# Kernel optimization log

Hardware: AMD Instinct MI355X
Metric: run time of the kernel (lower is better)

Reference implementation:

```python
import jax, jax.numpy as jnp
import numpy as np

GRID_SIZE, SPLINE_ORDER = 5, 3
NUM_BASES = GRID_SIZE + SPLINE_ORDER  # 8
GRID = jnp.asarray(np.arange(-SPLINE_ORDER, GRID_SIZE + SPLINE_ORDER + 1, dtype=np.float32) * (2.0 / GRID_SIZE) - 1.0)  # (12,)


def _b_splines(x):
    # x: (M, F) -> (M, F, NUM_BASES), Cox-de Boor recursion on shared uniform grid
    g = GRID
    xe = x[..., None]
    b = ((xe >= g[:-1]) & (xe < g[1:])).astype(x.dtype)
    for k in range(1, SPLINE_ORDER + 1):
        b = ((xe - g[:-(k + 1)]) / (g[k:-1] - g[:-(k + 1)]) * b[..., :-1]
             + (g[k + 1:] - xe) / (g[k + 1:] - g[1:-k]) * b[..., 1:])
    return b


def _kan_linear(x, base_w, spline_w):
    # x: (M, Fin); base_w: (Fout, Fin); spline_w: (Fout, Fin, NUM_BASES)
    base = jax.nn.silu(x) @ base_w.T
    spl = _b_splines(x).reshape(x.shape[0], -1) @ spline_w.reshape(spline_w.shape[0], -1).T
    return base + spl


def _ln(x, g, b, eps=1e-5):
    mu = jnp.mean(x, -1, keepdims=True)
    var = jnp.var(x, -1, keepdims=True)
    return (x - mu) * jax.lax.rsqrt(var + eps) * g + b


def _dwconv(img, w, b):
    C = img.shape[1]
    out = jax.lax.conv_general_dilated(img, w, (1, 1), 'SAME',
        dimension_numbers=('NCHW', 'OIHW', 'NCHW'), feature_group_count=C)
    return out + b[None, :, None, None]


def _dw_bn_relu(x, H, W, w, b, gamma, beta, eps=1e-5):
    # BN in eval mode with running_mean=0, running_var=1
    B, N, C = x.shape
    img = x.transpose(0, 2, 1).reshape(B, C, H, W)
    out = _dwconv(img, w, b)
    out = out * (gamma * (1.0 / np.sqrt(1.0 + eps)))[None, :, None, None] + beta[None, :, None, None]
    out = jax.nn.relu(out)
    return out.reshape(B, C, H * W).transpose(0, 2, 1)


def _cross_selective_scan(img, x_proj_w, dt_w, dt_b, A_logs, Ds, g, b):
    # img: (B, Di, H, W). 4-direction diagonal/antidiagonal selective scan (VMamba-style).
    B, Di, H, W = img.shape
    L = H * W
    K = x_proj_w.shape[0]
    R = dt_w.shape[2]
    Nst = A_logs.shape[1]
    i = jnp.arange(H)[:, None]
    j = jnp.arange(W)[None, :]
    diag = (i + j) % W
    adiag = (j - i) % W
    diag_inv = (jnp.arange(W)[None, :] - i) % W
    adiag_inv = (jnp.arange(W)[None, :] + i) % W

    def gather(x, idx):
        gth = jnp.take_along_axis(x, idx[None, None], axis=3)  # (B,Di,H,W)
        return gth.transpose(0, 1, 3, 2).reshape(B, Di, L)

    def scatter(flat, idx_inv):
        v = flat.reshape(B, Di, W, H).transpose(0, 1, 3, 2)
        return jnp.take_along_axis(v, idx_inv[None, None], axis=3)

    gd, gad = gather(img, diag), gather(img, adiag)
    xs = jnp.stack([gd, gad, jnp.flip(gd, -1), jnp.flip(gad, -1)], axis=1)  # (B,K,Di,L)
    x_dbl = jnp.einsum('bkdl,kcd->bkcl', xs, x_proj_w)
    dts, Bs, Cs = jnp.split(x_dbl, [R, R + Nst], axis=2)  # (B,K,R,L),(B,K,N,L),(B,K,N,L)
    dts = jnp.einsum('bkrl,kdr->bkdl', dts, dt_w)
    delta = jax.nn.softplus(dts + dt_b[None, :, :, None])  # (B,K,Di,L)
    A = -jnp.exp(A_logs).reshape(K, Di, Nst)

    def step(hst, inp):
        u_t, d_t, B_t, C_t = inp  # (B,K,Di),(B,K,Di),(B,K,N),(B,K,N)
        dA = jnp.exp(d_t[..., None] * A)
        hst = dA * hst + (d_t * u_t)[..., None] * B_t[:, :, None, :]
        return hst, jnp.einsum('bkdn,bkn->bkd', hst, C_t)

    h0 = jnp.zeros((B, K, Di, Nst), img.dtype)
    _, ys = jax.lax.scan(step, h0,
        (xs.transpose(3, 0, 1, 2), delta.transpose(3, 0, 1, 2),
         Bs.transpose(3, 0, 1, 2), Cs.transpose(3, 0, 1, 2)))  # ys: (L,B,K,Di)
    ys = ys.transpose(1, 2, 3, 0) + Ds.reshape(K, Di)[None, :, :, None] * xs  # (B,K,Di,L)
    yd = ys[:, 0] + jnp.flip(ys[:, 2], -1)
    ya = ys[:, 1] + jnp.flip(ys[:, 3], -1)
    y = scatter(yd, diag_inv) + scatter(ya, adiag_inv)  # (B,Di,H,W)
    y = y.reshape(B, Di, L).transpose(0, 2, 1)
    return _ln(y, g, b)  # (B,L,Di)


def setup_inputs():
    key = jax.random.key(0)
    ks = iter(jax.random.split(key, 48))
    B, H, W, C = 4, 64, 64, 96
    Di, K, Nst = 2 * C, 4, 16
    R = int(np.ceil(C / 16))
    L = H * W

    def rn(shape, s=0.05):
        return jax.random.normal(next(ks), shape, jnp.float32) * s

    return dict(
        x=jax.random.normal(next(ks), (B, L, C), jnp.float32),
        H=H, W=W,
        norm1_g=jnp.ones((C,), jnp.float32), norm1_b=jnp.zeros((C,), jnp.float32),
        in_proj_w=rn((2 * Di, C)),
        conv_w=rn((Di, 1, 3, 3), 0.2), conv_b=jnp.zeros((Di,), jnp.float32),
        x_proj_w=rn((K, R + 2 * Nst, Di)),
        dt_w=rn((K, Di, R), 0.1), dt_b=rn((K, Di), 0.1),
        A_logs=jax.random.uniform(next(ks), (K * Di, Nst), jnp.float32),
        Ds=jnp.ones((K * Di,), jnp.float32),
        out_norm_g=jnp.ones((Di,), jnp.float32), out_norm_b=jnp.zeros((Di,), jnp.float32),
        out_proj_w=rn((C, Di)),
        norm2_g=jnp.ones((C,), jnp.float32), norm2_b=jnp.zeros((C,), jnp.float32),
        fc1_base_w=rn((C, C)), fc1_spline_w=rn((C, C, NUM_BASES), 0.02),
        fc2_base_w=rn((C, C)), fc2_spline_w=rn((C, C, NUM_BASES), 0.02),
        fc3_base_w=rn((C, C)), fc3_spline_w=rn((C, C, NUM_BASES), 0.02),
        dw1_w=rn((C, 1, 3, 3), 0.2), dw1_b=jnp.zeros((C,), jnp.float32),
        dw1_g=jnp.ones((C,), jnp.float32), dw1_beta=jnp.zeros((C,), jnp.float32),
        dw2_w=rn((C, 1, 3, 3), 0.2), dw2_b=jnp.zeros((C,), jnp.float32),
        dw2_g=jnp.ones((C,), jnp.float32), dw2_beta=jnp.zeros((C,), jnp.float32),
        dw3_w=rn((C, 1, 3, 3), 0.2), dw3_b=jnp.zeros((C,), jnp.float32),
        dw3_g=jnp.ones((C,), jnp.float32), dw3_beta=jnp.zeros((C,), jnp.float32),
    )


def reference(x, H, W, norm1_g, norm1_b, in_proj_w, conv_w, conv_b, x_proj_w,
              dt_w, dt_b, A_logs, Ds, out_norm_g, out_norm_b, out_proj_w,
              norm2_g, norm2_b, fc1_base_w, fc1_spline_w, fc2_base_w, fc2_spline_w,
              fc3_base_w, fc3_spline_w, dw1_w, dw1_b, dw1_g, dw1_beta,
              dw2_w, dw2_b, dw2_g, dw2_beta, dw3_w, dw3_b, dw3_g, dw3_beta):
    B, L, C = x.shape
    # --- SS2D branch ---
    h = _ln(x, norm1_g, norm1_b)
    xz = h @ in_proj_w.T  # (B,L,2*Di)
    Di = xz.shape[-1] // 2
    xin, z = xz[..., :Di], xz[..., Di:]
    img = xin.transpose(0, 2, 1).reshape(B, Di, H, W)
    img = jax.nn.silu(_dwconv(img, conv_w, conv_b))
    y = _cross_selective_scan(img, x_proj_w, dt_w, dt_b, A_logs, Ds, out_norm_g, out_norm_b)
    y = y * jax.nn.silu(z)
    x = x + y @ out_proj_w.T
    # --- KAN branch ---
    h = _ln(x, norm2_g, norm2_b)
    M = B * L
    t = _kan_linear(h.reshape(M, C), fc1_base_w, fc1_spline_w).reshape(B, L, -1)
    t = _dw_bn_relu(t, H, W, dw1_w, dw1_b, dw1_g, dw1_beta)
    t = _kan_linear(t.reshape(M, -1), fc2_base_w, fc2_spline_w).reshape(B, L, -1)
    t = _dw_bn_relu(t, H, W, dw2_w, dw2_b, dw2_g, dw2_beta)
    t = _kan_linear(t.reshape(M, -1), fc3_base_w, fc3_spline_w).reshape(B, L, -1)
    t = _dw_bn_relu(t, H, W, dw3_w, dw3_b, dw3_g, dw3_beta)
    return x + t
```

## Files before the change

kernel.cpp:

```cpp
#include <hip/hip_runtime.h>
#include <math.h>

constexpr int B_  = 4;
constexpr int H_  = 64;
constexpr int W_  = 64;
constexpr int C_  = 96;
constexpr int L_  = H_ * W_;
constexpr int DI  = 192;
constexpr int K_  = 4;
constexpr int NST = 16;
constexpr int R_  = 6;
constexpr int M_  = B_ * L_;

constexpr int NCH = 128;
constexpr int CL  = 32;
constexpr int DG  = 12;

constexpr int KANK = 864;
constexpr int KLAY = 96 * KANK;

typedef __attribute__((ext_vector_type(8))) short short8;
typedef __attribute__((ext_vector_type(4))) float floatx4;
typedef __attribute__((ext_vector_type(4))) unsigned short ushort4v;

__device__ __forceinline__ float wave_sum64(float v) {
#pragma unroll
  for (int off = 1; off < 64; off <<= 1) v += __shfl_xor(v, off, 64);
  return v;
}

__device__ __forceinline__ float exp2_hw(float x) {
  return __builtin_amdgcn_exp2f(x);
}

__device__ __forceinline__ int pos_kl(int k, int l) {
  int ll = (k >= 2) ? (L_ - 1 - l) : l;
  int i = ll & 63;
  int j = ll >> 6;
  int col = ((k & 1) == 0) ? ((i + j) & 63) : ((j - i) & 63);
  return (i << 6) + col;
}

__device__ __forceinline__ int pos_pair(int pr, int ll) {
  int i = ll & 63, j = ll >> 6;
  int col = (pr == 0) ? ((i + j) & 63) : ((j - i) & 63);
  return (i << 6) + col;
}

__device__ __forceinline__ float silu_f(float x) {
  return x / (1.f + __expf(-x));
}

__device__ __forceinline__ float softplus_fast(float s) {
  return fmaxf(s, 0.f) + __logf(1.f + __expf(-fabsf(s)));
}

__device__ __forceinline__ unsigned short f2bf(float f) {
  unsigned u = __float_as_uint(f);
  unsigned r = (u + 0x7FFFu + ((u >> 16) & 1u)) >> 16;
  return (unsigned short)r;
}

__device__ __forceinline__ float bf2f(unsigned short h) {
  return __uint_as_float(((unsigned)h) << 16);
}

__device__ __forceinline__ void spline8(float x, float* bb ) {
#pragma unroll
  for (int i2 = 0; i2 < 11; i2++) {
    float g0 = 0.4f * i2 - 2.2f;
    float g1 = 0.4f * i2 - 1.8f;
    bb[i2] = (x >= g0 && x < g1) ? 1.f : 0.f;
  }
#pragma unroll
  for (int k2 = 1; k2 <= 3; k2++) {
    float invd = 1.f / (0.4f * k2);
#pragma unroll
    for (int i2 = 0; i2 + k2 < 11; i2++) {
      float gi   = 0.4f * i2 - 2.2f;
      float gik1 = 0.4f * (i2 + k2 + 1) - 2.2f;
      bb[i2] = (x - gi) * invd * bb[i2] + (gik1 - x) * invd * bb[i2 + 1];
    }
  }
}

__global__ __launch_bounds__(256) void ln96_kernel(const float* __restrict__ in,
    const float* __restrict__ g, const float* __restrict__ b,
    float* __restrict__ out) {
  int wave = blockIdx.x * 4 + (threadIdx.x >> 6);
  int lane = threadIdx.x & 63;
  const float* rp = in + (size_t)wave * C_;
  float v0 = rp[lane];
  float v1 = (lane < C_ - 64) ? rp[lane + 64] : 0.f;
  float s  = wave_sum64(v0 + v1);
  float s2 = wave_sum64(v0 * v0 + v1 * v1);
  float mean = s * (1.f / C_);
  float var  = s2 * (1.f / C_) - mean * mean;
  float inv  = rsqrtf(var + 1e-5f);
  float* op = out + (size_t)wave * C_;
  op[lane] = (v0 - mean) * inv * g[lane] + b[lane];
  if (lane < C_ - 64) op[lane + 64] = (v1 - mean) * inv * g[lane + 64] + b[lane + 64];
}

__global__ __launch_bounds__(256) void prep_inproj_kernel(const float* __restrict__ w,
    unsigned short* __restrict__ wio) {
  int idx = blockIdx.x * 256 + threadIdx.x;
  if (idx >= 384 * 96) return;
  float v = w[idx];
  unsigned short hh = f2bf(v);
  wio[idx] = hh;
  wio[36864 + idx] = f2bf(v - bf2f(hh));
}

__global__ __launch_bounds__(256) void prep_a2_kernel(const float* __restrict__ A_logs,
    float* __restrict__ a2g) {
  int idx = blockIdx.x * 256 + threadIdx.x;
  if (idx < K_ * DI * NST) a2g[idx] = -__expf(A_logs[idx]) * 1.44269504f;
}

__global__ __launch_bounds__(256) void gemm_in_mfma_kernel(const float* __restrict__ h,
    const unsigned short* __restrict__ wio, float* __restrict__ xin,
    float* __restrict__ z) {
  __shared__ __align__(16) unsigned short Wh[96][104];
  __shared__ __align__(16) unsigned short Wl[96][104];
  int row0 = blockIdx.x * 64;
  int tid = threadIdx.x;
  int wv = tid >> 6, lane = tid & 63, mrow = lane & 15, quad = lane >> 4;

  short8 ah[3], al[3];
  const float* hr = h + (size_t)(row0 + wv * 16 + mrow) * C_;
#pragma unroll
  for (int ks = 0; ks < 3; ks++) {
    float4 va = *(const float4*)&hr[ks * 32 + quad * 8];
    float4 vb = *(const float4*)&hr[ks * 32 + quad * 8 + 4];
    float f[8] = {va.x, va.y, va.z, va.w, vb.x, vb.y, vb.z, vb.w};
    short8 hh, ll;
#pragma unroll
    for (int q = 0; q < 8; q++) {
      unsigned short hv = f2bf(f[q]);
      hh[q] = (short)hv;
      ll[q] = (short)f2bf(f[q] - bf2f(hv));
    }
    ah[ks] = hh; al[ks] = ll;
  }
  for (int nc = 0; nc < 4; nc++) {
    if (nc) __syncthreads();
    for (int t = tid; t < 96 * 12; t += 256) {
      int j = t / 12, u = t % 12;
      *(short8*)&Wh[j][u * 8] = *(const short8*)&wio[(size_t)(nc * 96 + j) * 96 + u * 8];
      *(short8*)&Wl[j][u * 8] = *(const short8*)&wio[(size_t)(384 + nc * 96 + j) * 96 + u * 8];
    }
    __syncthreads();
    floatx4 acc[6];
#pragma unroll
    for (int q = 0; q < 6; q++) acc[q] = (floatx4)(0.f);
#pragma unroll
    for (int ks = 0; ks < 3; ks++) {
#pragma unroll
      for (int nt = 0; nt < 6; nt++) {
        short8 bh = *(const short8*)&Wh[nt * 16 + mrow][ks * 32 + quad * 8];
        short8 bl = *(const short8*)&Wl[nt * 16 + mrow][ks * 32 + quad * 8];
        acc[nt] = __builtin_amdgcn_mfma_f32_16x16x32_bf16(ah[ks], bh, acc[nt], 0, 0, 0);
        acc[nt] = __builtin_amdgcn_mfma_f32_16x16x32_bf16(al[ks], bh, acc[nt], 0, 0, 0);
        acc[nt] = __builtin_amdgcn_mfma_f32_16x16x32_bf16(ah[ks], bl, acc[nt], 0, 0, 0);
      }
    }
#pragma unroll
    for (int nt = 0; nt < 6; nt++) {
      int j = nc * 96 + nt * 16 + mrow;
#pragma unroll
      for (int rg = 0; rg < 4; rg++) {
        int row = row0 + wv * 16 + quad * 4 + rg;
        float v = acc[nt][rg];
        if (j < DI) xin[(size_t)row * DI + j] = v;
        else        z[(size_t)row * DI + (j - DI)] = v;
      }
    }
  }
}

__global__ __launch_bounds__(192) void conv_silu_kernel(const float* __restrict__ xin,
    const float* __restrict__ cw, const float* __restrict__ cb, float* __restrict__ imgT) {
  int p = blockIdx.x;
  int b = p >> 12;
  int ij = p & 4095;
  int i = ij >> 6, j = ij & 63;
  int c = threadIdx.x;
  float acc = cb[c];
#pragma unroll
  for (int di = -1; di <= 1; di++) {
    int ii = i + di;
    if (ii < 0 || ii >= H_) continue;
#pragma unroll
    for (int dj = -1; dj <= 1; dj++) {
      int jj = j + dj;
      if (jj < 0 || jj >= W_) continue;
      acc += xin[((size_t)b * L_ + ii * W_ + jj) * DI + c] * cw[c * 9 + (di + 1) * 3 + (dj + 1)];
    }
  }
  imgT[(size_t)p * DI + c] = silu_f(acc);
}

__global__ __launch_bounds__(256) void xdbl_mfma_kernel(const float* __restrict__ imgT,
    const float* __restrict__ xpw, float* __restrict__ dts_g,
    float* __restrict__ BsT, float* __restrict__ CsT) {
  __shared__ __align__(16) unsigned short Ah[64][104];
  __shared__ __align__(16) unsigned short Al[64][104];
  __shared__ __align__(16) unsigned short Wh[48][104];
  __shared__ __align__(16) unsigned short Wl[48][104];
  __shared__ int pos_s[64];

  int blk = blockIdx.x;
  int lt = blk & 63;
  int bk = blk >> 6;
  int k = bk % K_, b = bk / K_;
  int l0 = lt * 64;
  int tid = threadIdx.x;
  int wid = tid >> 6;
  int lane = tid & 63;
  int mrow = lane & 15, quad = lane >> 4;

  if (tid < 64) pos_s[tid] = pos_kl(k, l0 + tid);
  __syncthreads();

  floatx4 acc[3];
#pragma unroll
  for (int q = 0; q < 3; q++) acc[q] = (floatx4)(0.f);

  const float* img_b = imgT + (size_t)b * L_ * DI;
// ... 13 lines not shown
      }
      *(ushort4v*)&Ah[li][c4] = h4;
      *(ushort4v*)&Al[li][c4] = l4;
    }
    for (int t = tid; t < 48 * 24; t += 256) {
      int j = t / 24, c4 = (t % 24) * 4;
      ushort4v h4 = (ushort4v)0, l4 = (ushort4v)0;
      if (j < 38) {
        int c = (j < 32) ? (j + 6) : (j - 32);
        const float4 v = *(const float4*)&xpw[((size_t)(k * 38 + c)) * DI + kc * 96 + c4];
        float fv[4] = {v.x, v.y, v.z, v.w};
#pragma unroll
        for (int q = 0; q < 4; q++) {
          unsigned short hh = f2bf(fv[q]);
          h4[q] = hh;
          l4[q] = f2bf(fv[q] - bf2f(hh));
        }
      }
      *(ushort4v*)&Wh[j][c4] = h4;
      *(ushort4v*)&Wl[j][c4] = l4;
    }
    __syncthreads();
#pragma unroll
    for (int ks = 0; ks < 3; ks++) {
      short8 ah = *(const short8*)&Ah[wid * 16 + mrow][ks * 32 + quad * 8];
      short8 al = *(const short8*)&Al[wid * 16 + mrow][ks * 32 + quad * 8];
#pragma unroll
      for (int nt = 0; nt < 3; nt++) {
        short8 bh = *(const short8*)&Wh[nt * 16 + mrow][ks * 32 + quad * 8];
        short8 bl = *(const short8*)&Wl[nt * 16 + mrow][ks * 32 + quad * 8];
        acc[nt] = __builtin_amdgcn_mfma_f32_16x16x32_bf16(ah, bh, acc[nt], 0, 0, 0);
        acc[nt] = __builtin_amdgcn_mfma_f32_16x16x32_bf16(al, bh, acc[nt], 0, 0, 0);
        acc[nt] = __builtin_amdgcn_mfma_f32_16x16x32_bf16(ah, bl, acc[nt], 0, 0, 0);
      }
    }
  }
  size_t bkL = (size_t)(b * K_ + k) * L_ + l0;
#pragma unroll
  for (int rg = 0; rg < 4; rg++) {
    int grow = wid * 16 + quad * 4 + rg;
    size_t base = (bkL + grow) * NST;
    BsT[base + mrow] = acc[0][rg];
    CsT[base + mrow] = acc[1][rg];
    if (mrow < R_) dts_g[(bkL + grow) * 8 + mrow] = acc[2][rg];
  }
}

__global__ __launch_bounds__(192) void scan1_kernel(const float* __restrict__ imgT,
    const float* __restrict__ dts_g, const float* __restrict__ BsT,
    const float* __restrict__ a2g, const float* __restrict__ dtw,
    const float* __restrict__ dtb, float* __restrict__ hend,
    float* __restrict__ aprod) {
  __shared__ float bs_s[CL][NST];
  __shared__ float dt_s[CL][8];
  int blk = blockIdx.x;
  int c = blk % NCH;
  int tmp = blk / NCH;
  int k = tmp % K_, b = tmp / K_;
  int l0 = c * CL;
  int d = threadIdx.x;
  const float* img_b = imgT + (size_t)b * L_ * DI;
  {
    const float* Bs_bk = BsT + ((size_t)(b * K_ + k) * L_ + l0) * NST;
    for (int t = d; t < CL * NST; t += 192) bs_s[t >> 4][t & 15] = Bs_bk[t];
    const float* Dt = dts_g + ((size_t)(b * K_ + k) * L_ + l0) * 8;
    for (int t = d; t < CL * 8; t += 192) dt_s[t >> 3][t & 7] = Dt[t];
  }
  float A2[NST];
  {
    const floatx4* ap = (const floatx4*)(a2g + (size_t)(k * DI + d) * NST);
#pragma unroll
    for (int i = 0; i < 4; i++) {
      floatx4 v = ap[i];
      A2[4 * i] = v[0]; A2[4 * i + 1] = v[1]; A2[4 * i + 2] = v[2]; A2[4 * i + 3] = v[3];
    }
  }
  float w6[6], bias;
  {
    const float* wp = dtw + ((size_t)k * DI + d) * R_;
#pragma unroll
    for (int r = 0; r < 6; r++) w6[r] = wp[r];
    bias = dtb[k * DI + d];
  }
  float u[CL];
#pragma unroll
  for (int q = 0; q < CL; q++)
    u[q] = img_b[(size_t)pos_kl(k, l0 + q) * DI + d];
  __syncthreads();
  float dc[CL];
  float sum_dlt = 0.f;
#pragma unroll
  for (int q = 0; q < CL; q++) {
    const floatx4* dp = (const floatx4*)&dt_s[q][0];
    floatx4 d0 = dp[0], d1 = dp[1];
    float s = bias + w6[0] * d0[0] + w6[1] * d0[1] + w6[2] * d0[2]
                   + w6[3] * d0[3] + w6[4] * d1[0] + w6[5] * d1[1];
    dc[q] = softplus_fast(s);
    sum_dlt += dc[q];
  }
  float h[NST];
#pragma unroll
  for (int n = 0; n < NST; n++) h[n] = 0.f;
#pragma unroll
  for (int q = 0; q < CL; q++) {
    float du = dc[q] * u[q];
    floatx4 bsv[4];
    const floatx4* bp = (const floatx4*)&bs_s[q][0];
#pragma unroll
    for (int i = 0; i < 4; i++) bsv[i] = bp[i];
#pragma unroll
    for (int n = 0; n < NST; n++) {
      float dA = exp2_hw(dc[q] * A2[n]);
      h[n] = dA * h[n] + du * bsv[n >> 2][n & 3];
    }
  }
  size_t base = ((size_t)(b * K_ + k) * NCH + c) * (DI * NST) + d;
#pragma unroll
  for (int n = 0; n < NST; n++) {
    hend[base + (size_t)n * DI]  = h[n];
    aprod[base + (size_t)n * DI] = exp2_hw(A2[n] * sum_dlt);
  }
}

__global__ __launch_bounds__(256) void scan_carry_kernel(float* __restrict__ hend,
    const float* __restrict__ aprod) {
  constexpr int PF = 8;
  int blk = blockIdx.x;
  int part = blk % DG;
  int bk = blk / DG;
  const size_t DNS = (size_t)DI * NST;
  size_t base = (size_t)bk * NCH * DNS + (size_t)part * 256 + threadIdx.x;
  float hb[PF], ab[PF];
#pragma unroll
  for (int q = 0; q < PF; q++) {
    hb[q] = hend[base + (size_t)q * DNS];
    ab[q] = aprod[base + (size_t)q * DNS];
  }
  float carry = 0.f;
  for (int c0 = 0; c0 < NCH; c0 += PF) {
    float hn[PF], an[PF];
    if (c0 + PF < NCH) {
#pragma unroll
      for (int q = 0; q < PF; q++) {
        hn[q] = hend[base + (size_t)(c0 + PF + q) * DNS];
        an[q] = aprod[base + (size_t)(c0 + PF + q) * DNS];
      }
    } else {
#pragma unroll
      for (int q = 0; q < PF; q++) { hn[q] = 0.f; an[q] = 0.f; }
    }
#pragma unroll
    for (int q = 0; q < PF; q++) {
      hend[base + (size_t)(c0 + q) * DNS] = carry;
      carry = ab[q] * carry + hb[q];
    }
#pragma unroll
    for (int q = 0; q < PF; q++) { hb[q] = hn[q]; ab[q] = an[q]; }
  }
}

__global__ __launch_bounds__(192) void scan2_pair_kernel(const float* __restrict__ imgT,
    const float* __restrict__ dts_g, const float* __restrict__ BsT,
    const float* __restrict__ CsT, const float* __restrict__ a2g,
    const float* __restrict__ dtw, const float* __restrict__ dtb,
    const float* __restrict__ Ds, const float* __restrict__ carry_in,
    float* __restrict__ y02, float* __restrict__ y13) {
  __shared__ float bsf[CL][NST], csf[CL][NST], bsr[CL][NST], csr[CL][NST];
  __shared__ float dtf[CL][8], dtr[CL][8];
  int blk = blockIdx.x;
  int c  = blk % NCH;
  int pr = (blk / NCH) & 1;
  int b  = blk / (2 * NCH);
  int kf = pr, kr = pr + 2;
  int p0 = c * CL;
  int d = threadIdx.x;
  const float* img_b = imgT + (size_t)b * L_ * DI;
  {
    const float* Bf = BsT + ((size_t)(b * K_ + kf) * L_ + p0) * NST;
    const float* Cf = CsT + ((size_t)(b * K_ + kf) * L_ + p0) * NST;
    for (int t = d; t < CL * NST; t += 192) {
      bsf[t >> 4][t & 15] = Bf[t];
      csf[t >> 4][t & 15] = Cf[t];
    }
    const float* Br = BsT + (size_t)(b * K_ + kr) * L_ * NST;
    const float* Cr = CsT + (size_t)(b * K_ + kr) * L_ * NST;
    for (int t = d; t < CL * NST; t += 192) {
      int q = t >> 4, n = t & 15;
      size_t sr = (size_t)(L_ - 1 - p0 - q) * NST + n;
      bsr[q][n] = Br[sr];
      csr[q][n] = Cr[sr];
    }
    const float* Df = dts_g + ((size_t)(b * K_ + kf) * L_ + p0) * 8;
    for (int t = d; t < CL * 8; t += 192) dtf[t >> 3][t & 7] = Df[t];
    const float* Dr = dts_g + (size_t)(b * K_ + kr) * L_ * 8;
    for (int t = d; t < CL * 8; t += 192) {
      int q = t >> 3, r = t & 7;
      dtr[q][r] = Dr[(size_t)(L_ - 1 - p0 - q) * 8 + r];
    }
  }
  float u[CL], y[CL];
#pragma unroll
  for (int q = 0; q < CL; q++)
    u[q] = img_b[(size_t)pos_pair(pr, p0 + q) * DI + d];
  float dsum = 0.f;
  if (pr == 0) dsum = Ds[d] + Ds[DI + d] + Ds[2 * DI + d] + Ds[3 * DI + d];
#pragma unroll
  for (int q = 0; q < CL; q++) y[q] = dsum * u[q];
  __syncthreads();
  float A2[NST], h[NST], w6[6], bias, dc[CL];
  {
    const floatx4* ap = (const floatx4*)(a2g + (size_t)(kf * DI + d) * NST);
#pragma unroll
    for (int i = 0; i < 4; i++) {
      floatx4 v = ap[i];
      A2[4 * i] = v[0]; A2[4 * i + 1] = v[1]; A2[4 * i + 2] = v[2]; A2[4 * i + 3] = v[3];
    }
    size_t cb = ((size_t)(b * K_ + kf) * NCH + c) * (DI * NST) + d;
#pragma unroll
    for (int n = 0; n < NST; n++) h[n] = carry_in[cb + (size_t)n * DI];
    const float* wp = dtw + ((size_t)kf * DI + d) * R_;
#pragma unroll
    for (int r = 0; r < 6; r++) w6[r] = wp[r];
    bias = dtb[kf * DI + d];
  }
#pragma unroll
  for (int q = 0; q < CL; q++) {
    const floatx4* dp = (const floatx4*)&dtf[q][0];
    floatx4 d0 = dp[0], d1 = dp[1];
    float s = bias + w6[0] * d0[0] + w6[1] * d0[1] + w6[2] * d0[2]
                   + w6[3] * d0[3] + w6[4] * d1[0] + w6[5] * d1[1];
    dc[q] = softplus_fast(s);
  }
#pragma unroll
  for (int q = 0; q < CL; q++) {
    float du = dc[q] * u[q];
    floatx4 bsv[4], csv[4];
    const floatx4* bp = (const floatx4*)&bsf[q][0];
    const floatx4* cp = (const floatx4*)&csf[q][0];
#pragma unroll
    for (int i = 0; i < 4; i++) { bsv[i] = bp[i]; csv[i] = cp[i]; }
    float yq = y[q];
#pragma unroll
    for (int n = 0; n < NST; n++) {
      float dA = exp2_hw(dc[q] * A2[n]);
      h[n] = dA * h[n] + du * bsv[n >> 2][n & 3];
      yq += h[n] * csv[n >> 2][n & 3];
    }
    y[q] = yq;
  }
  {
    const floatx4* ap = (const floatx4*)(a2g + (size_t)(kr * DI + d) * NST);
#pragma unroll
    for (int i = 0; i < 4; i++) {
      floatx4 v = ap[i];
      A2[4 * i] = v[0]; A2[4 * i + 1] = v[1]; A2[4 * i + 2] = v[2]; A2[4 * i + 3] = v[3];
    }
    size_t cb = ((size_t)(b * K_ + kr) * NCH + (NCH - 1 - c)) * (DI * NST) + d;
#pragma unroll
    for (int n = 0; n < NST; n++) h[n] = carry_in[cb + (size_t)n * DI];
    const float* wp = dtw + ((size_t)kr * DI + d) * R_;
#pragma unroll
    for (int r = 0; r < 6; r++) w6[r] = wp[r];
    bias = dtb[kr * DI + d];
  }
#pragma unroll
  for (int q = 0; q < CL; q++) {
    const floatx4* dp = (const floatx4*)&dtr[q][0];
    floatx4 d0 = dp[0], d1 = dp[1];
    float s = bias + w6[0] * d0[0] + w6[1] * d0[1] + w6[2] * d0[2]
                   + w6[3] * d0[3] + w6[4] * d1[0] + w6[5] * d1[1];
    dc[q] = softplus_fast(s);
  }
#pragma unroll
  for (int qq = 0; qq < CL; qq++) {
    int q = CL - 1 - qq;
    float du = dc[q] * u[q];
    floatx4 bsv[4], csv[4];
    const floatx4* bp = (const floatx4*)&bsr[q][0];
    const floatx4* cp = (const floatx4*)&csr[q][0];
#pragma unroll
    for (int i = 0; i < 4; i++) { bsv[i] = bp[i]; csv[i] = cp[i]; }
    float yq = y[q];
#pragma unroll
    for (int n = 0; n < NST; n++) {
      float dA = exp2_hw(dc[q] * A2[n]);
      h[n] = dA * h[n] + du * bsv[n >> 2][n & 3];
      yq += h[n] * csv[n >> 2][n & 3];
    }
    y[q] = yq;
  }
  float* yout = (pr == 0) ? y02 : y13;
#pragma unroll
  for (int q = 0; q < CL; q++)
    yout[((size_t)b * L_ + pos_pair(pr, p0 + q)) * DI + d] = y[q];
}

__global__ __launch_bounds__(256) void ln_mulz_kernel(const float* __restrict__ y02,
    const float* __restrict__ y13, const float* __restrict__ g,
    const float* __restrict__ bb, float* __restrict__ z) {
  int wave = blockIdx.x * 4 + (threadIdx.x >> 6);
  int lane = threadIdx.x & 63;
  const float* rp = y02 + (size_t)wave * DI;
  const float* rq = y13 + (size_t)wave * DI;
  float v0 = rp[lane]       + rq[lane];
  float v1 = rp[lane + 64]  + rq[lane + 64];
  float v2 = rp[lane + 128] + rq[lane + 128];
  float s  = wave_sum64(v0 + v1 + v2);
  float s2 = wave_sum64(v0 * v0 + v1 * v1 + v2 * v2);
  float mean = s * (1.f / DI);
  float var  = s2 * (1.f / DI) - mean * mean;
  float inv  = rsqrtf(var + 1e-5f);
  float* zp = z + (size_t)wave * DI;
  float vv[3] = {v0, v1, v2};
#pragma unroll
  for (int q = 0; q < 3; q++) {
    int c = lane + 64 * q;
    float zv = zp[c];
    zp[c] = ((vv[q] - mean) * inv * g[c] + bb[c]) * silu_f(zv);
  }
}

__global__ __launch_bounds__(128) void outproj_kernel(const float* __restrict__ yz,
    const float* __restrict__ opw, const float* __restrict__ x, float* __restrict__ x_res) {
  __shared__ float ys[8][DI];
  int row0 = blockIdx.x * 8;
  for (int t = threadIdx.x; t < 8 * DI; t += 128)
    ys[t / DI][t % DI] = yz[(size_t)(row0 + t / DI) * DI + (t % DI)];
  __syncthreads();
  int j = threadIdx.x;
  if (j < C_) {
    float acc[8];
#pragma unroll
    for (int r = 0; r < 8; r++) acc[r] = 0.f;
    const float* wr = opw + (size_t)j * DI;
    for (int d = 0; d < DI; d++) {
      float wv = wr[d];
#pragma unroll
      for (int r = 0; r < 8; r++) acc[r] += wv * ys[r][d];
    }
#pragma unroll
    for (int r = 0; r < 8; r++) {
      size_t row = row0 + r;
      x_res[row * C_ + j] = x[row * C_ + j] + acc[r];
    }
  }
}

__global__ __launch_bounds__(256) void prepw_kernel(const float* __restrict__ bw1,
    const float* __restrict__ sw1, const float* __restrict__ bw2,
    const float* __restrict__ sw2, const float* __restrict__ bw3,
    const float* __restrict__ sw3, unsigned short* __restrict__ wcat) {
  int idx = blockIdx.x * 256 + threadIdx.x;
  if (idx >= 3 * KLAY) return;
  int layer = idx / KLAY, rem = idx % KLAY;
  int j = rem / KANK, k = rem % KANK;
  const float* bw = (layer == 0) ? bw1 : (layer == 1) ? bw2 : bw3;
  const float* sw = (layer == 0) ? sw1 : (layer == 1) ? sw2 : sw3;
  float v = (k < C_) ? bw[j * C_ + k] : sw[j * 768 + (k - C_)];
  wcat[idx] = f2bf(v);
}

__global__ __launch_bounds__(256) void kan_mfma_kernel(const float* __restrict__ in,
    const unsigned short* __restrict__ wl, float* __restrict__ out) {
  __shared__ __align__(16) float x_s[32][100];
  __shared__ __align__(16) unsigned short A_s[32][104];
  __shared__ __align__(16) unsigned short W_s[96][104];
  int row0 = blockIdx.x * 32;
  int tid = threadIdx.x;
  for (int t = tid; t < 32 * 24; t += 256) {
    int r = t / 24, c4 = (t % 24) * 4;
    *(float4*)&x_s[r][c4] = *(const float4*)&in[(size_t)(row0 + r) * C_ + c4];
  }
  floatx4 acc[3];
#pragma unroll
  for (int q = 0; q < 3; q++) acc[q] = (floatx4)(0.f);
  int wv = tid >> 6;
  int rh = wv >> 1, ch = wv & 1;
  int lane = tid & 63;
  int mrow = lane & 15, quad = lane >> 4;
  __syncthreads();
  for (int ci = 0; ci < 9; ci++) {
    if (ci) __syncthreads();
    for (int t = tid; t < 96 * 12; t += 256) {
      int j = t / 12, u = t % 12;
      *(short8*)&W_s[j][u * 8] =
          *(const short8*)&wl[(size_t)j * KANK + ci * 96 + u * 8];
    }
    if (ci == 0) {
      for (int t = tid; t < 32 * 48; t += 256) {
        int r = t / 48, k2 = (t % 48) * 2;
        unsigned v = (unsigned)f2bf(silu_f(x_s[r][k2])) |
                     ((unsigned)f2bf(silu_f(x_s[r][k2 + 1])) << 16);
        *(unsigned*)&A_s[r][k2] = v;
      }
    } else {
      int c0 = (ci - 1) * 12;
      for (int t = tid; t < 32 * 12; t += 256) {
        int r = t & 31, cl = t >> 5;
        float x = x_s[r][c0 + cl];
        float bb[11];
        spline8(x, bb);
// ... 26 lines not shown
__global__ __launch_bounds__(192) void dwbn_kernel(const float* __restrict__ t,
    const float* __restrict__ w, const float* __restrict__ bias,
    const float* __restrict__ gamma, const float* __restrict__ beta,
    const float* __restrict__ addres, float* __restrict__ out) {
  int tid = threadIdx.x;
  int half = (tid >= 96) ? 1 : 0;
  int c = tid - half * 96;
  int p = blockIdx.x * 2 + half;
  int b = p >> 12;
  int ij = p & 4095;
  int i = ij >> 6, j = ij & 63;
  float acc = bias[c];
#pragma unroll
  for (int di = -1; di <= 1; di++) {
    int ii = i + di;
    if (ii < 0 || ii >= H_) continue;
#pragma unroll
    for (int dj = -1; dj <= 1; dj++) {
      int jj = j + dj;
      if (jj < 0 || jj >= W_) continue;
      acc += t[((size_t)b * L_ + ii * W_ + jj) * C_ + c] * w[c * 9 + (di + 1) * 3 + (dj + 1)];
    }
  }
  float v = acc * (gamma[c] * rsqrtf(1.f + 1e-5f)) + beta[c];
  v = fmaxf(v, 0.f);
  if (addres != nullptr) v += addres[(size_t)p * C_ + c];
  out[(size_t)p * C_ + c] = v;
}

extern "C" void kernel_launch(void* const* d_in, const int* in_sizes, int n_in,
                              void* d_out, int out_size, void* d_ws, size_t ws_size,
                              hipStream_t stream) {
  const float* x         = (const float*)d_in[0];
  const float* norm1_g   = (const float*)d_in[3];
  const float* norm1_b   = (const float*)d_in[4];
  const float* in_proj_w = (const float*)d_in[5];
  const float* conv_w    = (const float*)d_in[6];
  const float* conv_b    = (const float*)d_in[7];
  const float* x_proj_w  = (const float*)d_in[8];
  const float* dt_w      = (const float*)d_in[9];
  const float* dt_b      = (const float*)d_in[10];
  const float* A_logs    = (const float*)d_in[11];
  const float* Ds        = (const float*)d_in[12];
  const float* out_ng    = (const float*)d_in[13];
  const float* out_nb    = (const float*)d_in[14];
  const float* out_proj_w= (const float*)d_in[15];
  const float* norm2_g   = (const float*)d_in[16];
  const float* norm2_b   = (const float*)d_in[17];
  const float* fc1_bw    = (const float*)d_in[18];
  const float* fc1_sw    = (const float*)d_in[19];
  const float* fc2_bw    = (const float*)d_in[20];
  const float* fc2_sw    = (const float*)d_in[21];
  const float* fc3_bw    = (const float*)d_in[22];
  const float* fc3_sw    = (const float*)d_in[23];
  const float* dw1_w     = (const float*)d_in[24];
  const float* dw1_b     = (const float*)d_in[25];
  const float* dw1_g     = (const float*)d_in[26];
  const float* dw1_be    = (const float*)d_in[27];
  const float* dw2_w     = (const float*)d_in[28];
  const float* dw2_b     = (const float*)d_in[29];
  const float* dw2_g     = (const float*)d_in[30];
  const float* dw2_be    = (const float*)d_in[31];
  const float* dw3_w     = (const float*)d_in[32];
  const float* dw3_b     = (const float*)d_in[33];
  const float* dw3_g     = (const float*)d_in[34];
  const float* dw3_be    = (const float*)d_in[35];

  float* ws = (float*)d_ws;
  float* h_buf   = ws;
  float* xin_buf = h_buf + (size_t)M_ * C_;
  float* z_buf   = xin_buf + (size_t)M_ * DI;
  float* imgT    = z_buf + (size_t)M_ * DI;
  float* BsT     = imgT + (size_t)M_ * DI;
  float* CsT     = BsT + (size_t)B_ * K_ * L_ * NST;
  float* y_pre   = CsT + (size_t)B_ * K_ * L_ * NST;
  float* x_res   = y_pre + (size_t)M_ * DI;
  float* t_a     = x_res + (size_t)M_ * C_;
  float* t_b     = t_a + (size_t)M_ * C_;
  float* hend    = t_b + (size_t)M_ * C_;
  float* aprod   = hend + (size_t)B_ * K_ * NCH * DI * NST;
  float* a2_buf  = aprod + (size_t)B_ * K_ * NCH * DI * NST;
  float* dts_g   = t_a;
  unsigned short* wio  = (unsigned short*)t_b;
  float* y13     = xin_buf;
  unsigned short* wcat = (unsigned short*)BsT;

  ln96_kernel<<<M_ / 4, 256, 0, stream>>>(x, norm1_g, norm1_b, h_buf);
  prep_inproj_kernel<<<144, 256, 0, stream>>>(in_proj_w, wio);
  prep_a2_kernel<<<48, 256, 0, stream>>>(A_logs, a2_buf);
  gemm_in_mfma_kernel<<<M_ / 64, 256, 0, stream>>>(h_buf, wio, xin_buf, z_buf);
  conv_silu_kernel<<<M_, 192, 0, stream>>>(xin_buf, conv_w, conv_b, imgT);
  xdbl_mfma_kernel<<<B_ * K_ * (L_ / 64), 256, 0, stream>>>(imgT, x_proj_w, dts_g,
                                                            BsT, CsT);
  scan1_kernel<<<B_ * K_ * NCH, 192, 0, stream>>>(imgT, dts_g, BsT, a2_buf,
                                                  dt_w, dt_b, hend, aprod);
  scan_carry_kernel<<<B_ * K_ * DG, 256, 0, stream>>>(hend, aprod);
  scan2_pair_kernel<<<B_ * 2 * NCH, 192, 0, stream>>>(imgT, dts_g, BsT, CsT, a2_buf,
                                                      dt_w, dt_b, Ds, hend,
                                                      y_pre, y13);
  prepw_kernel<<<(3 * KLAY + 255) / 256, 256, 0, stream>>>(fc1_bw, fc1_sw, fc2_bw,
                                                           fc2_sw, fc3_bw, fc3_sw, wcat);
  ln_mulz_kernel<<<M_ / 4, 256, 0, stream>>>(y_pre, y13, out_ng, out_nb, z_buf);
  outproj_kernel<<<M_ / 8, 128, 0, stream>>>(z_buf, out_proj_w, x, x_res);
  ln96_kernel<<<M_ / 4, 256, 0, stream>>>(x_res, norm2_g, norm2_b, h_buf);
  kan_mfma_kernel<<<M_ / 32, 256, 0, stream>>>(h_buf, wcat, t_a);
  dwbn_kernel<<<M_ / 2, 192, 0, stream>>>(t_a, dw1_w, dw1_b, dw1_g, dw1_be, nullptr, t_b);
  kan_mfma_kernel<<<M_ / 32, 256, 0, stream>>>(t_b, wcat + KLAY, t_a);
  dwbn_kernel<<<M_ / 2, 192, 0, stream>>>(t_a, dw2_w, dw2_b, dw2_g, dw2_be, nullptr, t_b);
  kan_mfma_kernel<<<M_ / 32, 256, 0, stream>>>(t_b, wcat + 2 * KLAY, t_a);
  dwbn_kernel<<<M_ / 2, 192, 0, stream>>>(t_a, dw3_w, dw3_b, dw3_g, dw3_be, x_res, (float*)d_out);
}
```

Before: 489.5 us.

## Sub-block scan loops to cut registers and split input GEMM across column halves

The scan1 and scan2 kernels now walk each 32-step chunk in sub-blocks of 8 with a prefetch of the next sub-block's inputs, instead of holding all 32 u, dt and y values in registers. scan2 keeps forward-pass partial outputs in a new LDS buffer instead of registers. The aim is lower VGPR pressure and higher occupancy, at the cost of more LDS use per block and LDS reads in the inner loop. Separately, the input-projection GEMM launches twice as many blocks, each covering half of the output columns, for more parallelism, though each block re-converts its A tile.

```diff
diff --git a/kernel.cpp b/kernel.cpp
--- a/kernel.cpp
+++ b/kernel.cpp
@@ -15,6 +15,7 @@
 constexpr int NCH = 128;
 constexpr int CL  = 32;
 constexpr int DG  = 12;
+constexpr int SB  = 8;
 
 constexpr int KANK = 864;
 constexpr int KLAY = 96 * KANK;
@@ -123,7 +124,8 @@
     float* __restrict__ z) {
   __shared__ __align__(16) unsigned short Wh[96][104];
   __shared__ __align__(16) unsigned short Wl[96][104];
-  int row0 = blockIdx.x * 64;
+  int row0 = (blockIdx.x >> 1) * 64;
+  int nc0  = (blockIdx.x & 1) * 2;
   int tid = threadIdx.x;
   int wv = tid >> 6, lane = tid & 63, mrow = lane & 15, quad = lane >> 4;
 
@@ -143,8 +145,9 @@
     }
     ah[ks] = hh; al[ks] = ll;
   }
-  for (int nc = 0; nc < 4; nc++) {
-    if (nc) __syncthreads();
+  for (int nci = 0; nci < 2; nci++) {
+    int nc = nc0 + nci;
+    if (nci) __syncthreads();
     for (int t = tid; t < 96 * 12; t += 256) {
       int j = t / 12, u = t % 12;
       *(short8*)&Wh[j][u * 8] = *(const short8*)&wio[(size_t)(nc * 96 + j) * 96 + u * 8];
@@ -324,36 +327,46 @@
     for (int r = 0; r < 6; r++) w6[r] = wp[r];
     bias = dtb[k * DI + d];
   }
-  float u[CL];
-#pragma unroll
-  for (int q = 0; q < CL; q++)
-    u[q] = img_b[(size_t)pos_kl(k, l0 + q) * DI + d];
+  float u_cur[SB];
+#pragma unroll
+  for (int t = 0; t < SB; t++)
+    u_cur[t] = img_b[(size_t)pos_kl(k, l0 + t) * DI + d];
   __syncthreads();
-  float dc[CL];
+  float h[NST];
+#pragma unroll
+  for (int n = 0; n < NST; n++) h[n] = 0.f;
   float sum_dlt = 0.f;
-#pragma unroll
-  for (int q = 0; q < CL; q++) {
-    const floatx4* dp = (const floatx4*)&dt_s[q][0];
-    floatx4 d0 = dp[0], d1 = dp[1];
-    float s = bias + w6[0] * d0[0] + w6[1] * d0[1] + w6[2] * d0[2]
-                   + w6[3] * d0[3] + w6[4] * d1[0] + w6[5] * d1[1];
-    dc[q] = softplus_fast(s);
-    sum_dlt += dc[q];
-  }
-  float h[NST];
-#pragma unroll
-  for (int n = 0; n < NST; n++) h[n] = 0.f;
-#pragma unroll
-  for (int q = 0; q < CL; q++) {
-    float du = dc[q] * u[q];
-    floatx4 bsv[4];
-    const floatx4* bp = (const floatx4*)&bs_s[q][0];
-#pragma unroll
-    for (int i = 0; i < 4; i++) bsv[i] = bp[i];
-#pragma unroll
-    for (int n = 0; n < NST; n++) {
-      float dA = exp2_hw(dc[q] * A2[n]);
-      h[n] = dA * h[n] + du * bsv[n >> 2][n & 3];
+#pragma unroll 1
+  for (int sb = 0; sb < CL / SB; sb++) {
+    float u_nxt[SB];
+    if (sb + 1 < CL / SB) {
+#pragma unroll
+      for (int t = 0; t < SB; t++)
+        u_nxt[t] = img_b[(size_t)pos_kl(k, l0 + (sb + 1) * SB + t) * DI + d];
+    }
+    float dc8[SB];
+#pragma unroll
+    for (int t = 0; t < SB; t++) {
+      const floatx4* dp = (const floatx4*)&dt_s[sb * SB + t][0];
+      floatx4 d0 = dp[0], d1 = dp[1];
+      float s = bias + w6[0] * d0[0] + w6[1] * d0[1] + w6[2] * d0[2]
+                     + w6[3] * d0[3] + w6[4] * d1[0] + w6[5] * d1[1];
+      dc8[t] = softplus_fast(s);
+      sum_dlt += dc8[t];
+    }
+#pragma unroll
+    for (int t = 0; t < SB; t++) {
+      int q = sb * SB + t;
+      float du = dc8[t] * u_cur[t];
+#pragma unroll
+      for (int n = 0; n < NST; n++) {
+        float dA = exp2_hw(dc8[t] * A2[n]);
+        h[n] = dA * h[n] + du * bs_s[q][n];
+      }
+    }
+    if (sb + 1 < CL / SB) {
+#pragma unroll
+      for (int t = 0; t < SB; t++) u_cur[t] = u_nxt[t];
     }
   }
   size_t base = ((size_t)(b * K_ + k) * NCH + c) * (DI * NST) + d;
@@ -409,6 +422,7 @@
     float* __restrict__ y02, float* __restrict__ y13) {
   __shared__ float bsf[CL][NST], csf[CL][NST], bsr[CL][NST], csr[CL][NST];
   __shared__ float dtf[CL][8], dtr[CL][8];
+  __shared__ float y_lds[CL][DI];
   int blk = blockIdx.x;
   int c  = blk % NCH;
   int pr = (blk / NCH) & 1;
@@ -440,16 +454,9 @@
       dtr[q][r] = Dr[(size_t)(L_ - 1 - p0 - q) * 8 + r];
     }
   }
-  float u[CL], y[CL];
-#pragma unroll
-  for (int q = 0; q < CL; q++)
-    u[q] = img_b[(size_t)pos_pair(pr, p0 + q) * DI + d];
   float dsum = 0.f;
   if (pr == 0) dsum = Ds[d] + Ds[DI + d] + Ds[2 * DI + d] + Ds[3 * DI + d];
-#pragma unroll
-  for (int q = 0; q < CL; q++) y[q] = dsum * u[q];
-  __syncthreads();
-  float A2[NST], h[NST], w6[6], bias, dc[CL];
+  float A2[NST], h[NST], w6[6], bias;
   {
     const floatx4* ap = (const floatx4*)(a2g + (size_t)(kf * DI + d) * NST);
 #pragma unroll
@@ -465,30 +472,45 @@
     for (int r = 0; r < 6; r++) w6[r] = wp[r];
     bias = dtb[kf * DI + d];
   }
-#pragma unroll
-  for (int q = 0; q < CL; q++) {
-    const floatx4* dp = (const floatx4*)&dtf[q][0];
-    floatx4 d0 = dp[0], d1 = dp[1];
-    float s = bias + w6[0] * d0[0] + w6[1] * d0[1] + w6[2] * d0[2]
-                   + w6[3] * d0[3] + w6[4] * d1[0] + w6[5] * d1[1];
-    dc[q] = softplus_fast(s);
-  }
-#pragma unroll
-  for (int q = 0; q < CL; q++) {
-    float du = dc[q] * u[q];
-    floatx4 bsv[4], csv[4];
-    const floatx4* bp = (const floatx4*)&bsf[q][0];
-    const floatx4* cp = (const floatx4*)&csf[q][0];
-#pragma unroll
-    for (int i = 0; i < 4; i++) { bsv[i] = bp[i]; csv[i] = cp[i]; }
-    float yq = y[q];
-#pragma unroll
-    for (int n = 0; n < NST; n++) {
-      float dA = exp2_hw(dc[q] * A2[n]);
-      h[n] = dA * h[n] + du * bsv[n >> 2][n & 3];
-      yq += h[n] * csv[n >> 2][n & 3];
-    }
-    y[q] = yq;
+  float u_cur[SB];
+#pragma unroll
+  for (int t = 0; t < SB; t++)
+    u_cur[t] = img_b[(size_t)pos_pair(pr, p0 + t) * DI + d];
+  __syncthreads();
+#pragma unroll 1
+  for (int sb = 0; sb < CL / SB; sb++) {
+    float u_nxt[SB];
+    if (sb + 1 < CL / SB) {
+#pragma unroll
+      for (int t = 0; t < SB; t++)
+        u_nxt[t] = img_b[(size_t)pos_pair(pr, p0 + (sb + 1) * SB + t) * DI + d];
+    }
+    float dc8[SB];
+#pragma unroll
+    for (int t = 0; t < SB; t++) {
+      const floatx4* dp = (const floatx4*)&dtf[sb * SB + t][0];
+      floatx4 d0 = dp[0], d1 = dp[1];
+      float s = bias + w6[0] * d0[0] + w6[1] * d0[1] + w6[2] * d0[2]
+                     + w6[3] * d0[3] + w6[4] * d1[0] + w6[5] * d1[1];
+      dc8[t] = softplus_fast(s);
+    }
+#pragma unroll
+    for (int t = 0; t < SB; t++) {
+      int q = sb * SB + t;
+      float du = dc8[t] * u_cur[t];
+      float yq = dsum * u_cur[t];
+#pragma unroll
+      for (int n = 0; n < NST; n++) {
+        float dA = exp2_hw(dc8[t] * A2[n]);
+        h[n] = dA * h[n] + du * bsf[q][n];
+        yq += h[n] * csf[q][n];
+      }
+      y_lds[q][d] = yq;
+    }
+    if (sb + 1 < CL / SB) {
+#pragma unroll
+      for (int t = 0; t < SB; t++) u_cur[t] = u_nxt[t];
+    }
   }
   {
     const floatx4* ap = (const floatx4*)(a2g + (size_t)(kr * DI + d) * NST);
@@ -505,36 +527,45 @@
     for (int r = 0; r < 6; r++) w6[r] = wp[r];
     bias = dtb[kr * DI + d];
   }
-#pragma unroll
-  for (int q = 0; q < CL; q++) {
-    const floatx4* dp = (const floatx4*)&dtr[q][0];
-    floatx4 d0 = dp[0], d1 = dp[1];
-    float s = bias + w6[0] * d0[0] + w6[1] * d0[1] + w6[2] * d0[2]
-                   + w6[3] * d0[3] + w6[4] * d1[0] + w6[5] * d1[1];
-    dc[q] = softplus_fast(s);
-  }
-#pragma unroll
-  for (int qq = 0; qq < CL; qq++) {
-    int q = CL - 1 - qq;
-    float du = dc[q] * u[q];
-    floatx4 bsv[4], csv[4];
-    const floatx4* bp = (const floatx4*)&bsr[q][0];
-    const floatx4* cp = (const floatx4*)&csr[q][0];
-#pragma unroll
-    for (int i = 0; i < 4; i++) { bsv[i] = bp[i]; csv[i] = cp[i]; }
-    float yq = y[q];
-#pragma unroll
-    for (int n = 0; n < NST; n++) {
-      float dA = exp2_hw(dc[q] * A2[n]);
-      h[n] = dA * h[n] + du * bsv[n >> 2][n & 3];
-      yq += h[n] * csv[n >> 2][n & 3];
-    }
-    y[q] = yq;
-  }
   float* yout = (pr == 0) ? y02 : y13;
 #pragma unroll
-  for (int q = 0; q < CL; q++)
-    yout[((size_t)b * L_ + pos_pair(pr, p0 + q)) * DI + d] = y[q];
+  for (int t = 0; t < SB; t++)
+    u_cur[t] = img_b[(size_t)pos_pair(pr, p0 + (CL - SB) + t) * DI + d];
+#pragma unroll 1
+  for (int sb = CL / SB - 1; sb >= 0; sb--) {
+    float u_nxt[SB];
+    if (sb > 0) {
+#pragma unroll
+      for (int t = 0; t < SB; t++)
+        u_nxt[t] = img_b[(size_t)pos_pair(pr, p0 + (sb - 1) * SB + t) * DI + d];
+    }
+    float dc8[SB];
+#pragma unroll
+    for (int t = 0; t < SB; t++) {
+      const floatx4* dp = (const floatx4*)&dtr[sb * SB + t][0];
+      floatx4 d0 = dp[0], d1 = dp[1];
+      float s = bias + w6[0] * d0[0] + w6[1] * d0[1] + w6[2] * d0[2]
+                     + w6[3] * d0[3] + w6[4] * d1[0] + w6[5] * d1[1];
+      dc8[t] = softplus_fast(s);
+    }
+#pragma unroll
+    for (int tt = SB - 1; tt >= 0; tt--) {
+      int q = sb * SB + tt;
+      float du = dc8[tt] * u_cur[tt];
+      float yq = y_lds[q][d];
+#pragma unroll
+      for (int n = 0; n < NST; n++) {
+        float dA = exp2_hw(dc8[tt] * A2[n]);
+        h[n] = dA * h[n] + du * bsr[q][n];
+        yq += h[n] * csr[q][n];
+      }
+      yout[((size_t)b * L_ + pos_pair(pr, p0 + q)) * DI + d] = yq;
+    }
+    if (sb > 0) {
+#pragma unroll
+      for (int t = 0; t < SB; t++) u_cur[t] = u_nxt[t];
+    }
+  }
 }
 
 __global__ __launch_bounds__(256) void ln_mulz_kernel(const float* __restrict__ y02,
@@ -757,7 +788,7 @@
   ln96_kernel<<<M_ / 4, 256, 0, stream>>>(x, norm1_g, norm1_b, h_buf);
   prep_inproj_kernel<<<144, 256, 0, stream>>>(in_proj_w, wio);
   prep_a2_kernel<<<48, 256, 0, stream>>>(A_logs, a2_buf);
-  gemm_in_mfma_kernel<<<M_ / 64, 256, 0, stream>>>(h_buf, wio, xin_buf, z_buf);
+  gemm_in_mfma_kernel<<<(M_ / 64) * 2, 256, 0, stream>>>(h_buf, wio, xin_buf, z_buf);
   conv_silu_kernel<<<M_, 192, 0, stream>>>(xin_buf, conv_w, conv_b, imgT);
   xdbl_mfma_kernel<<<B_ * K_ * (L_ / 64), 256, 0, stream>>>(imgT, x_proj_w, dts_g,
                                                             BsT, CsT);
```

Result: no change. 499.0 us (+1.9%).

## Split scan2 over state halves and in-proj GEMM over column halves for more blocks

Applied to the files above, without the earlier changes.

The second-pass scan kernel now splits the 16 SSM states into two halves of 8, doubling the grid and halving per-thread state registers and shared memory. Partial outputs go to four separate buffers, one reusing the aprod region, and the LN/mul-z kernel sums all four. The in-projection GEMM also splits each row tile's four column chunks across two blocks, doubling its grid. The aim is more parallelism and occupancy, at the cost of recomputing dt/softplus and rereading inputs per half plus extra output traffic.

```diff
diff --git a/kernel.cpp b/kernel.cpp
--- a/kernel.cpp
+++ b/kernel.cpp
@@ -15,6 +15,7 @@
 constexpr int NCH = 128;
 constexpr int CL  = 32;
 constexpr int DG  = 12;
+constexpr int HS  = 8;
 
 constexpr int KANK = 864;
 constexpr int KLAY = 96 * KANK;
@@ -123,7 +124,8 @@
     float* __restrict__ z) {
   __shared__ __align__(16) unsigned short Wh[96][104];
   __shared__ __align__(16) unsigned short Wl[96][104];
-  int row0 = blockIdx.x * 64;
+  int row0 = (blockIdx.x >> 1) * 64;
+  int nc0  = (blockIdx.x & 1) * 2;
   int tid = threadIdx.x;
   int wv = tid >> 6, lane = tid & 63, mrow = lane & 15, quad = lane >> 4;
 
@@ -143,8 +145,9 @@
     }
     ah[ks] = hh; al[ks] = ll;
   }
-  for (int nc = 0; nc < 4; nc++) {
-    if (nc) __syncthreads();
+  for (int nci = 0; nci < 2; nci++) {
+    int nc = nc0 + nci;
+    if (nci) __syncthreads();
     for (int t = tid; t < 96 * 12; t += 256) {
       int j = t / 12, u = t % 12;
       *(short8*)&Wh[j][u * 8] = *(const short8*)&wio[(size_t)(nc * 96 + j) * 96 + u * 8];
@@ -401,34 +404,39 @@
   }
 }
 
-__global__ __launch_bounds__(192) void scan2_pair_kernel(const float* __restrict__ imgT,
+__global__ __launch_bounds__(192) void scan2_quad_kernel(const float* __restrict__ imgT,
     const float* __restrict__ dts_g, const float* __restrict__ BsT,
     const float* __restrict__ CsT, const float* __restrict__ a2g,
     const float* __restrict__ dtw, const float* __restrict__ dtb,
     const float* __restrict__ Ds, const float* __restrict__ carry_in,
-    float* __restrict__ y02, float* __restrict__ y13) {
-  __shared__ float bsf[CL][NST], csf[CL][NST], bsr[CL][NST], csr[CL][NST];
+    float* __restrict__ y0g, float* __restrict__ y1g,
+    float* __restrict__ y2g, float* __restrict__ y3g) {
+  __shared__ float bsf[CL][HS], csf[CL][HS], bsr[CL][HS], csr[CL][HS];
   __shared__ float dtf[CL][8], dtr[CL][8];
   int blk = blockIdx.x;
-  int c  = blk % NCH;
-  int pr = (blk / NCH) & 1;
-  int b  = blk / (2 * NCH);
+  int c    = blk % NCH;
+  int rest = blk / NCH;
+  int pr = rest & 1;
+  int hf = (rest >> 1) & 1;
+  int b  = rest >> 2;
   int kf = pr, kr = pr + 2;
+  int n0 = hf * HS;
   int p0 = c * CL;
   int d = threadIdx.x;
   const float* img_b = imgT + (size_t)b * L_ * DI;
   {
     const float* Bf = BsT + ((size_t)(b * K_ + kf) * L_ + p0) * NST;
     const float* Cf = CsT + ((size_t)(b * K_ + kf) * L_ + p0) * NST;
-    for (int t = d; t < CL * NST; t += 192) {
-      bsf[t >> 4][t & 15] = Bf[t];
-      csf[t >> 4][t & 15] = Cf[t];
+    for (int t = d; t < CL * HS; t += 192) {
+      int q = t >> 3, n = t & 7;
+      bsf[q][n] = Bf[q * NST + n0 + n];
+      csf[q][n] = Cf[q * NST + n0 + n];
     }
     const float* Br = BsT + (size_t)(b * K_ + kr) * L_ * NST;
     const float* Cr = CsT + (size_t)(b * K_ + kr) * L_ * NST;
-    for (int t = d; t < CL * NST; t += 192) {
-      int q = t >> 4, n = t & 15;
-      size_t sr = (size_t)(L_ - 1 - p0 - q) * NST + n;
+    for (int t = d; t < CL * HS; t += 192) {
+      int q = t >> 3, n = t & 7;
+      size_t sr = (size_t)(L_ - 1 - p0 - q) * NST + n0 + n;
       bsr[q][n] = Br[sr];
       csr[q][n] = Cr[sr];
     }
@@ -445,21 +453,19 @@
   for (int q = 0; q < CL; q++)
     u[q] = img_b[(size_t)pos_pair(pr, p0 + q) * DI + d];
   float dsum = 0.f;
-  if (pr == 0) dsum = Ds[d] + Ds[DI + d] + Ds[2 * DI + d] + Ds[3 * DI + d];
+  if (pr == 0 && hf == 0)
+    dsum = Ds[d] + Ds[DI + d] + Ds[2 * DI + d] + Ds[3 * DI + d];
 #pragma unroll
   for (int q = 0; q < CL; q++) y[q] = dsum * u[q];
   __syncthreads();
-  float A2[NST], h[NST], w6[6], bias, dc[CL];
+  float A2[HS], h[HS], w6[6], bias, dc[CL];
   {
-    const floatx4* ap = (const floatx4*)(a2g + (size_t)(kf * DI + d) * NST);
-#pragma unroll
-    for (int i = 0; i < 4; i++) {
-      floatx4 v = ap[i];
-      A2[4 * i] = v[0]; A2[4 * i + 1] = v[1]; A2[4 * i + 2] = v[2]; A2[4 * i + 3] = v[3];
-    }
-    size_t cb = ((size_t)(b * K_ + kf) * NCH + c) * (DI * NST) + d;
-#pragma unroll
-    for (int n = 0; n < NST; n++) h[n] = carry_in[cb + (size_t)n * DI];
+    const float* ap = a2g + (size_t)(kf * DI + d) * NST + n0;
+#pragma unroll
+    for (int n = 0; n < HS; n++) A2[n] = ap[n];
+    size_t cb = ((size_t)(b * K_ + kf) * NCH + c) * (DI * NST) + (size_t)n0 * DI + d;
+#pragma unroll
+    for (int n = 0; n < HS; n++) h[n] = carry_in[cb + (size_t)n * DI];
     const float* wp = dtw + ((size_t)kf * DI + d) * R_;
 #pragma unroll
     for (int r = 0; r < 6; r++) w6[r] = wp[r];
@@ -476,30 +482,23 @@
 #pragma unroll
   for (int q = 0; q < CL; q++) {
     float du = dc[q] * u[q];
-    floatx4 bsv[4], csv[4];
-    const floatx4* bp = (const floatx4*)&bsf[q][0];
-    const floatx4* cp = (const floatx4*)&csf[q][0];
-#pragma unroll
-    for (int i = 0; i < 4; i++) { bsv[i] = bp[i]; csv[i] = cp[i]; }
     float yq = y[q];
 #pragma unroll
-    for (int n = 0; n < NST; n++) {
+    for (int n = 0; n < HS; n++) {
       float dA = exp2_hw(dc[q] * A2[n]);
-      h[n] = dA * h[n] + du * bsv[n >> 2][n & 3];
-      yq += h[n] * csv[n >> 2][n & 3];
+      h[n] = dA * h[n] + du * bsf[q][n];
+      yq += h[n] * csf[q][n];
     }
     y[q] = yq;
   }
   {
-    const floatx4* ap = (const floatx4*)(a2g + (size_t)(kr * DI + d) * NST);
-#pragma unroll
-    for (int i = 0; i < 4; i++) {
-      floatx4 v = ap[i];
-      A2[4 * i] = v[0]; A2[4 * i + 1] = v[1]; A2[4 * i + 2] = v[2]; A2[4 * i + 3] = v[3];
-    }
-    size_t cb = ((size_t)(b * K_ + kr) * NCH + (NCH - 1 - c)) * (DI * NST) + d;
-#pragma unroll
-    for (int n = 0; n < NST; n++) h[n] = carry_in[cb + (size_t)n * DI];
+    const float* ap = a2g + (size_t)(kr * DI + d) * NST + n0;
+#pragma unroll
+    for (int n = 0; n < HS; n++) A2[n] = ap[n];
+    size_t cb = ((size_t)(b * K_ + kr) * NCH + (NCH - 1 - c)) * (DI * NST)
+                + (size_t)n0 * DI + d;
+#pragma unroll
+    for (int n = 0; n < HS; n++) h[n] = carry_in[cb + (size_t)n * DI];
     const float* wp = dtw + ((size_t)kr * DI + d) * R_;
 #pragma unroll
     for (int r = 0; r < 6; r++) w6[r] = wp[r];
@@ -517,48 +516,45 @@
   for (int qq = 0; qq < CL; qq++) {
     int q = CL - 1 - qq;
     float du = dc[q] * u[q];
-    floatx4 bsv[4], csv[4];
-    const floatx4* bp = (const floatx4*)&bsr[q][0];
-    const floatx4* cp = (const floatx4*)&csr[q][0];
-#pragma unroll
-    for (int i = 0; i < 4; i++) { bsv[i] = bp[i]; csv[i] = cp[i]; }
     float yq = y[q];
 #pragma unroll
-    for (int n = 0; n < NST; n++) {
+    for (int n = 0; n < HS; n++) {
       float dA = exp2_hw(dc[q] * A2[n]);
-      h[n] = dA * h[n] + du * bsv[n >> 2][n & 3];
-      yq += h[n] * csv[n >> 2][n & 3];
+      h[n] = dA * h[n] + du * bsr[q][n];
+      yq += h[n] * csr[q][n];
     }
     y[q] = yq;
   }
-  float* yout = (pr == 0) ? y02 : y13;
+  float* yout = (hf == 0) ? ((pr == 0) ? y0g : y1g) : ((pr == 0) ? y2g : y3g);
 #pragma unroll
   for (int q = 0; q < CL; q++)
     yout[((size_t)b * L_ + pos_pair(pr, p0 + q)) * DI + d] = y[q];
 }
 
-__global__ __launch_bounds__(256) void ln_mulz_kernel(const float* __restrict__ y02,
-    const float* __restrict__ y13, const float* __restrict__ g,
+__global__ __launch_bounds__(256) void ln_mulz_kernel(const float* __restrict__ y0g,
+    const float* __restrict__ y1g, const float* __restrict__ y2g,
+    const float* __restrict__ y3g, const float* __restrict__ g,
     const float* __restrict__ bb, float* __restrict__ z) {
   int wave = blockIdx.x * 4 + (threadIdx.x >> 6);
   int lane = threadIdx.x & 63;
-  const float* rp = y02 + (size_t)wave * DI;
-  const float* rq = y13 + (size_t)wave * DI;
-  float v0 = rp[lane]       + rq[lane];
-  float v1 = rp[lane + 64]  + rq[lane + 64];
-  float v2 = rp[lane + 128] + rq[lane + 128];
-  float s  = wave_sum64(v0 + v1 + v2);
-  float s2 = wave_sum64(v0 * v0 + v1 * v1 + v2 * v2);
+  size_t base = (size_t)wave * DI;
+  float v[3];
+#pragma unroll
+  for (int q = 0; q < 3; q++) {
+    size_t idx = base + lane + 64 * q;
+    v[q] = y0g[idx] + y1g[idx] + y2g[idx] + y3g[idx];
+  }
+  float s  = wave_sum64(v[0] + v[1] + v[2]);
+  float s2 = wave_sum64(v[0] * v[0] + v[1] * v[1] + v[2] * v[2]);
   float mean = s * (1.f / DI);
   float var  = s2 * (1.f / DI) - mean * mean;
   float inv  = rsqrtf(var + 1e-5f);
-  float* zp = z + (size_t)wave * DI;
-  float vv[3] = {v0, v1, v2};
+  float* zp = z + base;
 #pragma unroll
   for (int q = 0; q < 3; q++) {
     int c = lane + 64 * q;
     float zv = zp[c];
-    zp[c] = ((vv[q] - mean) * inv * g[c] + bb[c]) * silu_f(zv);
+    zp[c] = ((v[q] - mean) * inv * g[c] + bb[c]) * silu_f(zv);
   }
 }
 
@@ -751,25 +747,28 @@
   float* a2_buf  = aprod + (size_t)B_ * K_ * NCH * DI * NST;
   float* dts_g   = t_a;
   unsigned short* wio  = (unsigned short*)t_b;
-  float* y13     = xin_buf;
+  float* y1_buf  = xin_buf;
+  float* y2_buf  = aprod;
+  float* y3_buf  = aprod + (size_t)M_ * DI;
   unsigned short* wcat = (unsigned short*)BsT;
 
   ln96_kernel<<<M_ / 4, 256, 0, stream>>>(x, norm1_g, norm1_b, h_buf);
   prep_inproj_kernel<<<144, 256, 0, stream>>>(in_proj_w, wio);
   prep_a2_kernel<<<48, 256, 0, stream>>>(A_logs, a2_buf);
-  gemm_in_mfma_kernel<<<M_ / 64, 256, 0, stream>>>(h_buf, wio, xin_buf, z_buf);
+  gemm_in_mfma_kernel<<<(M_ / 64) * 2, 256, 0, stream>>>(h_buf, wio, xin_buf, z_buf);
   conv_silu_kernel<<<M_, 192, 0, stream>>>(xin_buf, conv_w, conv_b, imgT);
   xdbl_mfma_kernel<<<B_ * K_ * (L_ / 64), 256, 0, stream>>>(imgT, x_proj_w, dts_g,
                                                             BsT, CsT);
   scan1_kernel<<<B_ * K_ * NCH, 192, 0, stream>>>(imgT, dts_g, BsT, a2_buf,
                                                   dt_w, dt_b, hend, aprod);
   scan_carry_kernel<<<B_ * K_ * DG, 256, 0, stream>>>(hend, aprod);
-  scan2_pair_kernel<<<B_ * 2 * NCH, 192, 0, stream>>>(imgT, dts_g, BsT, CsT, a2_buf,
+  scan2_quad_kernel<<<B_ * 4 * NCH, 192, 0, stream>>>(imgT, dts_g, BsT, CsT, a2_buf,
                                                       dt_w, dt_b, Ds, hend,
-                                                      y_pre, y13);
+                                                      y_pre, y1_buf, y2_buf, y3_buf);
   prepw_kernel<<<(3 * KLAY + 255) / 256, 256, 0, stream>>>(fc1_bw, fc1_sw, fc2_bw,
                                                            fc2_sw, fc3_bw, fc3_sw, wcat);
-  ln_mulz_kernel<<<M_ / 4, 256, 0, stream>>>(y_pre, y13, out_ng, out_nb, z_buf);
+  ln_mulz_kernel<<<M_ / 4, 256, 0, stream>>>(y_pre, y1_buf, y2_buf, y3_buf,
+                                             out_ng, out_nb, z_buf);
   outproj_kernel<<<M_ / 8, 128, 0, stream>>>(z_buf, out_proj_w, x, x_res);
   ln96_kernel<<<M_ / 4, 256, 0, stream>>>(x_res, norm2_g, norm2_b, h_buf);
   kan_mfma_kernel<<<M_ / 32, 256, 0, stream>>>(h_buf, wcat, t_a);
```

Result: no change. 493.2 us (+0.8%).
